# Optimization experiments

Hardware: AMD Instinct MI355X
Metric: run time of the kernel (lower is better)

Reference implementation:

```python
import jax, jax.numpy as jnp
import numpy as np

DIM = 512
T = 65536


def setup_inputs() -> dict:
    key = jax.random.key(0)
    k1, = jax.random.split(key, 1)
    z_rest = jax.random.normal(k1, (T, DIM), dtype=jnp.float32)
    # var_vbl = inv_softplus(sqrt(var_init)) with var_init=1.0 -> log(expm1(1.0))
    var_vbl = jnp.full((DIM,), float(np.log(np.expm1(1.0))), dtype=jnp.float32)
    # corr_vbl = inv_sigmoid(0.1) = log(0.1) - log(0.9)
    corr_vbl = jnp.full((DIM,), float(np.log(0.1) - np.log(0.9)), dtype=jnp.float32)
    prior_mu = jnp.zeros((DIM,), dtype=jnp.float32)
    return {"z_rest": z_rest, "var_vbl": var_vbl, "corr_vbl": corr_vbl, "prior_mu": prior_mu}


def reference(z_rest, var_vbl, corr_vbl, prior_mu):
    # init_train_lkd with z_context=None, starting from fresh state (sample_size=0).
    prior_var = jnp.square(jax.nn.softplus(var_vbl))          # [D]
    prior_cov = jax.nn.sigmoid(corr_vbl) * prior_var          # [D]
    two_pi = 2.0 * jnp.pi

    def step(carry, xs):
        mu, var, lkd = carry
        z, t = xs  # z: [D], t: scalar step index (== sample_size - 1 after increment)
        lkd = lkd + jnp.sum(-0.5 * jnp.log(two_pi * var)
                            - jnp.square(z - mu) / (2.0 * var))
        dd = prior_cov / (prior_var + prior_cov * t)
        mu = (1.0 - dd) * mu + z * dd
        var = (1.0 - dd) * var + (prior_var - prior_cov) * dd
        return (mu, var, lkd), None

    ts = jnp.arange(z_rest.shape[0], dtype=z_rest.dtype)
    init = (prior_mu.astype(z_rest.dtype), prior_var, jnp.zeros((), z_rest.dtype))
    (_, _, lkd), _ = jax.lax.scan(step, init, (z_rest, ts))
    return lkd
```

## Files before the change

### kernel.cpp

```cpp
#include <hip/hip_runtime.h>
#include <math.h>


#define DIM    512
#define TT     65536
#define CHUNKS 1024
#define ROWS   64
#define GROUPS 64
#define CPG    16

#define TWO_PI 6.283185307179586

__global__ __launch_bounds__(128) void k1_colsum(const float* __restrict__ z,
                                                 float* __restrict__ sums) {
    const int chunk = blockIdx.x;
    const int tid = threadIdx.x;
    const float4* zp = reinterpret_cast<const float4*>(z)
                       + (size_t)chunk * ROWS * (DIM / 4) + tid;
    float sx = 0.f, sy = 0.f, szs = 0.f, sw = 0.f;
#pragma unroll 16
    for (int r = 0; r < ROWS; ++r) {
        float4 v = zp[(size_t)r * (DIM / 4)];
        sx += v.x; sy += v.y; szs += v.z; sw += v.w;
    }
    reinterpret_cast<float4*>(sums)[(size_t)chunk * (DIM / 4) + tid]
        = make_float4(sx, sy, szs, sw);
}

__global__ __launch_bounds__(512) void k2a_scan(float* __restrict__ sums,
                                                float* __restrict__ gsums) {
    const int g = blockIdx.x;
    const int d = threadIdx.x;
    float vals[CPG];
#pragma unroll
    for (int i = 0; i < CPG; ++i)
        vals[i] = sums[(size_t)(g * CPG + i) * DIM + d];
    float run = 0.f;
#pragma unroll
    for (int i = 0; i < CPG; ++i) {
        sums[(size_t)(g * CPG + i) * DIM + d] = run;
        run += vals[i];
    }
    gsums[(size_t)g * DIM + d] = run;
}

__global__ __launch_bounds__(512) void k2b_scan(float* __restrict__ gsums,
                                                const float* __restrict__ var_vbl,
                                                const float* __restrict__ corr_vbl,
                                                float* __restrict__ out) {
    const int d = threadIdx.x;
    float vals[GROUPS];
#pragma unroll
    for (int g = 0; g < GROUPS; ++g)
        vals[g] = gsums[(size_t)g * DIM + d];
    float run = 0.f;
#pragma unroll
    for (int g = 0; g < GROUPS; ++g) {
        gsums[(size_t)g * DIM + d] = run;
        run += vals[g];
    }
    double sp = log1p(exp((double)var_vbl[d]));
    double v = sp * sp;
    double cc = v / (1.0 + exp(-(double)corr_vbl[d]));
    double vmc = v - cc;
    double Dlast = v + cc * (double)(TT - 1);
    double Ld = -0.5 * ((double)TT * (log(TWO_PI) + log(vmc)) + log(Dlast / vmc));
    __shared__ double red[512];
    red[d] = Ld;
    __syncthreads();
    for (int s = 256; s > 0; s >>= 1) {
        if (d < s) red[d] += red[d + s];
        __syncthreads();
    }
    if (d == 0) atomicAdd(out, (float)red[0]);
}

__global__ __launch_bounds__(128) void k3_main(const float* __restrict__ z,
                                               const float* __restrict__ sums,
                                               const float* __restrict__ gsums,
                                               const float* __restrict__ var_vbl,
                                               const float* __restrict__ corr_vbl,
                                               const float* __restrict__ prior_mu,
                                               float* __restrict__ out) {
    const int chunk = blockIdx.x;
    const int tid = threadIdx.x;
    const int d0 = tid * 4;
    const int g = chunk / CPG;
    const float t0m1 = (float)(chunk * ROWS) - 1.0f;

    float vv[4], cc[4], k0[4], kq[4], Z[4], Dprev[4], invDprev[4];
#pragma unroll
    for (int j = 0; j < 4; ++j) {
        const int d = d0 + j;
        float spv = log1pf(expf(var_vbl[d]));
        float v = spv * spv;
        float c = v / (1.0f + expf(-corr_vbl[d]));
        float vmc = v - c;
        vv[j] = v;
        cc[j] = c;
        k0[j] = vmc * prior_mu[d];
        kq[j] = 0.5f / vmc;
        Z[j] = sums[(size_t)chunk * DIM + d] + gsums[(size_t)g * DIM + d];
        Dprev[j] = fmaf(c, t0m1, v);
        invDprev[j] = __builtin_amdgcn_rcpf(Dprev[j]);
    }

    const float4* zp = reinterpret_cast<const float4*>(z)
                       + (size_t)chunk * ROWS * (DIM / 4) + tid;
    float acc = 0.f;
    float tf = t0m1 + 1.0f;
#pragma unroll 4
    for (int r = 0; r < ROWS; ++r) {
        float4 zv = zp[(size_t)r * (DIM / 4)];
        float zz[4] = {zv.x, zv.y, zv.z, zv.w};
#pragma unroll
        for (int j = 0; j < 4; ++j) {
            float Dt = fmaf(cc[j], tf, vv[j]);
            float invDt = __builtin_amdgcn_rcpf(Dt);
            float mu = fmaf(cc[j], Z[j], k0[j]) * invDprev[j];
            float e = zz[j] - mu;
            acc = fmaf(e * e * Dprev[j] * invDt, kq[j], acc);
            Z[j] += zz[j];
            Dprev[j] = Dt;
            invDprev[j] = invDt;
        }
        tf += 1.0f;
    }

    for (int off = 32; off > 0; off >>= 1) acc += __shfl_down(acc, off, 64);
    __shared__ float wsred[2];
    const int lane = tid & 63, w = tid >> 6;
    if (lane == 0) wsred[w] = acc;
    __syncthreads();
    if (tid == 0) atomicAdd(out, -(wsred[0] + wsred[1]));
}

extern "C" void kernel_launch(void* const* d_in, const int* in_sizes, int n_in,
                              void* d_out, int out_size, void* d_ws, size_t ws_size,
                              hipStream_t stream) {
    const float* z = (const float*)d_in[0];
    const float* var_vbl = (const float*)d_in[1];
    const float* corr_vbl = (const float*)d_in[2];
    const float* prior_mu = (const float*)d_in[3];
    float* out = (float*)d_out;
    float* sums = (float*)d_ws;
    float* gsums = sums + (size_t)CHUNKS * DIM;

    hipMemsetAsync(d_out, 0, sizeof(float), stream);
    k1_colsum<<<CHUNKS, 128, 0, stream>>>(z, sums);
    k2a_scan<<<GROUPS, 512, 0, stream>>>(sums, gsums);
    k2b_scan<<<1, 512, 0, stream>>>(gsums, var_vbl, corr_vbl, out);
    k3_main<<<CHUNKS, 128, 0, stream>>>(z, sums, gsums, var_vbl, corr_vbl,
                                        prior_mu, out);
}
```

Before: 235.4 us.

## Single-pass over z using per-chunk quadratic moments instead of second read

The quadratic likelihood term is expanded algebraically so that each chunk accumulates local moments (S0, S1, S2) relative to the chunk-local prefix sum. A small combine kernel then applies the global prefix offset per chunk. This removes the second full pass over the 128 MB input and the memset, at the cost of extra workspace writes and float32 cancellation risk in the expanded quadratic form.

```diff
diff --git a/kernel.cpp b/kernel.cpp
--- a/kernel.cpp
+++ b/kernel.cpp
@@ -11,23 +11,66 @@
 
 #define TWO_PI 6.283185307179586
 
-__global__ __launch_bounds__(128) void k1_colsum(const float* __restrict__ z,
-                                                 float* __restrict__ sums) {
+__global__ __launch_bounds__(128) void k1_fused(const float* __restrict__ z,
+                                                const float* __restrict__ var_vbl,
+                                                const float* __restrict__ corr_vbl,
+                                                const float* __restrict__ prior_mu,
+                                                float* __restrict__ sums,
+                                                float* __restrict__ s0a,
+                                                float* __restrict__ s1a,
+                                                float* __restrict__ s2a) {
     const int chunk = blockIdx.x;
     const int tid = threadIdx.x;
+    const int d0 = tid * 4;
+    const float t0m1 = (float)(chunk * ROWS) - 1.0f;
+
+    float vv[4], cc[4], k0[4], L[4], S0[4], S1[4], S2[4], Dprev[4], invDprev[4];
+#pragma unroll
+    for (int j = 0; j < 4; ++j) {
+        const int d = d0 + j;
+        float spv = log1pf(expf(var_vbl[d]));
+        float v = spv * spv;
+        float c = v / (1.0f + expf(-corr_vbl[d]));
+        vv[j] = v;
+        cc[j] = c;
+        k0[j] = (v - c) * prior_mu[d];
+        L[j] = 0.f; S0[j] = 0.f; S1[j] = 0.f; S2[j] = 0.f;
+        Dprev[j] = fmaf(c, t0m1, v);
+        invDprev[j] = __builtin_amdgcn_rcpf(Dprev[j]);
+    }
+
     const float4* zp = reinterpret_cast<const float4*>(z)
                        + (size_t)chunk * ROWS * (DIM / 4) + tid;
-    float sx = 0.f, sy = 0.f, szs = 0.f, sw = 0.f;
-#pragma unroll 16
+    float tf = t0m1 + 1.0f;
+#pragma unroll 4
     for (int r = 0; r < ROWS; ++r) {
-        float4 v = zp[(size_t)r * (DIM / 4)];
-        sx += v.x; sy += v.y; szs += v.z; sw += v.w;
+        float4 zv = zp[(size_t)r * (DIM / 4)];
+        float zz[4] = {zv.x, zv.y, zv.z, zv.w};
+#pragma unroll
+        for (int j = 0; j < 4; ++j) {
+            float Dt = fmaf(cc[j], tf, vv[j]);
+            float invDt = __builtin_amdgcn_rcpf(Dt);
+            float w = fmaf(Dprev[j], zz[j], -fmaf(cc[j], L[j], k0[j]));
+            float rr = invDt * invDprev[j];
+            S0[j] += rr;
+            float rw = rr * w;
+            S1[j] += rw;
+            S2[j] = fmaf(rw, w, S2[j]);
+            L[j] += zz[j];
+            Dprev[j] = Dt;
+            invDprev[j] = invDt;
+        }
+        tf += 1.0f;
     }
-    reinterpret_cast<float4*>(sums)[(size_t)chunk * (DIM / 4) + tid]
-        = make_float4(sx, sy, szs, sw);
+
+    const size_t o4 = (size_t)chunk * (DIM / 4) + tid;
+    reinterpret_cast<float4*>(sums)[o4] = make_float4(L[0], L[1], L[2], L[3]);
+    reinterpret_cast<float4*>(s0a)[o4] = make_float4(S0[0], S0[1], S0[2], S0[3]);
+    reinterpret_cast<float4*>(s1a)[o4] = make_float4(S1[0], S1[1], S1[2], S1[3]);
+    reinterpret_cast<float4*>(s2a)[o4] = make_float4(S2[0], S2[1], S2[2], S2[3]);
 }
 
-__global__ __launch_bounds__(512) void k2a_scan(float* __restrict__ sums,
+__global__ __launch_bounds__(512) void k2a_gsum(const float* __restrict__ sums,
                                                 float* __restrict__ gsums) {
     const int g = blockIdx.x;
     const int d = threadIdx.x;
@@ -37,10 +80,7 @@
         vals[i] = sums[(size_t)(g * CPG + i) * DIM + d];
     float run = 0.f;
 #pragma unroll
-    for (int i = 0; i < CPG; ++i) {
-        sums[(size_t)(g * CPG + i) * DIM + d] = run;
-        run += vals[i];
-    }
+    for (int i = 0; i < CPG; ++i) run += vals[i];
     gsums[(size_t)g * DIM + d] = run;
 }
 
@@ -72,67 +112,49 @@
         if (d < s) red[d] += red[d + s];
         __syncthreads();
     }
-    if (d == 0) atomicAdd(out, (float)red[0]);
+    if (d == 0) out[0] = (float)red[0];
 }
 
-__global__ __launch_bounds__(128) void k3_main(const float* __restrict__ z,
-                                               const float* __restrict__ sums,
-                                               const float* __restrict__ gsums,
-                                               const float* __restrict__ var_vbl,
-                                               const float* __restrict__ corr_vbl,
-                                               const float* __restrict__ prior_mu,
-                                               float* __restrict__ out) {
-    const int chunk = blockIdx.x;
-    const int tid = threadIdx.x;
-    const int d0 = tid * 4;
-    const int g = chunk / CPG;
-    const float t0m1 = (float)(chunk * ROWS) - 1.0f;
+__global__ __launch_bounds__(512) void k2c_combine(const float* __restrict__ sums,
+                                                   const float* __restrict__ gsums,
+                                                   const float* __restrict__ s0a,
+                                                   const float* __restrict__ s1a,
+                                                   const float* __restrict__ s2a,
+                                                   const float* __restrict__ var_vbl,
+                                                   const float* __restrict__ corr_vbl,
+                                                   float* __restrict__ out) {
+    const int g = blockIdx.x;
+    const int d = threadIdx.x;
+    float spv = log1pf(expf(var_vbl[d]));
+    float v = spv * spv;
+    float c = v / (1.0f + expf(-corr_vbl[d]));
+    float kq = 0.5f / (v - c);
 
-    float vv[4], cc[4], k0[4], kq[4], Z[4], Dprev[4], invDprev[4];
+    float run = gsums[(size_t)g * DIM + d];
+    float q = 0.f;
 #pragma unroll
-    for (int j = 0; j < 4; ++j) {
-        const int d = d0 + j;
-        float spv = log1pf(expf(var_vbl[d]));
-        float v = spv * spv;
-        float c = v / (1.0f + expf(-corr_vbl[d]));
-        float vmc = v - c;
-        vv[j] = v;
-        cc[j] = c;
-        k0[j] = vmc * prior_mu[d];
-        kq[j] = 0.5f / vmc;
-        Z[j] = sums[(size_t)chunk * DIM + d] + gsums[(size_t)g * DIM + d];
-        Dprev[j] = fmaf(c, t0m1, v);
-        invDprev[j] = __builtin_amdgcn_rcpf(Dprev[j]);
+    for (int i = 0; i < CPG; ++i) {
+        const size_t idx = (size_t)(g * CPG + i) * DIM + d;
+        float s = sums[idx];
+        float S0 = s0a[idx];
+        float S1 = s1a[idx];
+        float S2 = s2a[idx];
+        float cP = c * run;
+        q += kq * (S2 - 2.f * cP * S1 + cP * cP * S0);
+        run += s;
     }
 
-    const float4* zp = reinterpret_cast<const float4*>(z)
-                       + (size_t)chunk * ROWS * (DIM / 4) + tid;
-    float acc = 0.f;
-    float tf = t0m1 + 1.0f;
-#pragma unroll 4
-    for (int r = 0; r < ROWS; ++r) {
-        float4 zv = zp[(size_t)r * (DIM / 4)];
-        float zz[4] = {zv.x, zv.y, zv.z, zv.w};
+    for (int off = 32; off > 0; off >>= 1) q += __shfl_down(q, off, 64);
+    __shared__ float wsred[8];
+    const int lane = d & 63, w = d >> 6;
+    if (lane == 0) wsred[w] = q;
+    __syncthreads();
+    if (d == 0) {
+        float tot = 0.f;
 #pragma unroll
-        for (int j = 0; j < 4; ++j) {
-            float Dt = fmaf(cc[j], tf, vv[j]);
-            float invDt = __builtin_amdgcn_rcpf(Dt);
-            float mu = fmaf(cc[j], Z[j], k0[j]) * invDprev[j];
-            float e = zz[j] - mu;
-            acc = fmaf(e * e * Dprev[j] * invDt, kq[j], acc);
-            Z[j] += zz[j];
-            Dprev[j] = Dt;
-            invDprev[j] = invDt;
-        }
-        tf += 1.0f;
+        for (int i = 0; i < 8; ++i) tot += wsred[i];
+        atomicAdd(out, -tot);
     }
-
-    for (int off = 32; off > 0; off >>= 1) acc += __shfl_down(acc, off, 64);
-    __shared__ float wsred[2];
-    const int lane = tid & 63, w = tid >> 6;
-    if (lane == 0) wsred[w] = acc;
-    __syncthreads();
-    if (tid == 0) atomicAdd(out, -(wsred[0] + wsred[1]));
 }
 
 extern "C" void kernel_launch(void* const* d_in, const int* in_sizes, int n_in,
@@ -144,12 +166,15 @@
     const float* prior_mu = (const float*)d_in[3];
     float* out = (float*)d_out;
     float* sums = (float*)d_ws;
-    float* gsums = sums + (size_t)CHUNKS * DIM;
+    float* s0a = sums + (size_t)CHUNKS * DIM;
+    float* s1a = s0a + (size_t)CHUNKS * DIM;
+    float* s2a = s1a + (size_t)CHUNKS * DIM;
+    float* gsums = s2a + (size_t)CHUNKS * DIM;
 
-    hipMemsetAsync(d_out, 0, sizeof(float), stream);
-    k1_colsum<<<CHUNKS, 128, 0, stream>>>(z, sums);
-    k2a_scan<<<GROUPS, 512, 0, stream>>>(sums, gsums);
+    k1_fused<<<CHUNKS, 128, 0, stream>>>(z, var_vbl, corr_vbl, prior_mu,
+                                         sums, s0a, s1a, s2a);
+    k2a_gsum<<<GROUPS, 512, 0, stream>>>(sums, gsums);
     k2b_scan<<<1, 512, 0, stream>>>(gsums, var_vbl, corr_vbl, out);
-    k3_main<<<CHUNKS, 128, 0, stream>>>(z, sums, gsums, var_vbl, corr_vbl,
-                                        prior_mu, out);
+    k2c_combine<<<GROUPS, 512, 0, stream>>>(sums, gsums, s0a, s1a, s2a,
+                                            var_vbl, corr_vbl, out);
 }
```

Measured after the change: 207.2 us. 12.0% less time.
